# Kernel optimization log

Hardware: AMD Instinct MI355X
Metric: run time of the kernel (lower is better)

## Reference

```python
import jax, jax.numpy as jnp
import numpy as np

B, C_IN, N_NODES = 128, 64, 1024
N_TRIPLES = 3 * (N_NODES - 1)  # node 0 is the shared zero vector


def _btc(x, idx, w, b):
    # x: [B, C, N]; idx: [B, 3M]; w: [O, C, 3]; b: [O]
    Bv, C, _ = x.shape
    T = idx.shape[1]
    g = jnp.take_along_axis(x, jnp.broadcast_to(idx[:, None, :], (Bv, C, T)), axis=2)
    g = g.reshape(Bv, C, T // 3, 3)  # stride-3 kernel-3 conv == per-triple contraction
    out = jnp.einsum('bcnk,ock->bon', g, w) + b[None, :, None]
    zero = jnp.zeros((Bv, out.shape[1], 1), dtype=out.dtype)
    return jnp.concatenate([zero, out], axis=2)  # re-prepend zero node -> [B, O, N]


def _tln(x):
    mean = jnp.mean(x, axis=(1, 2), keepdims=True)
    std = jnp.std(x, axis=(1, 2), ddof=1, keepdims=True)  # torch.std is unbiased
    return (x - mean) / (std + 1e-5)


def _tower(x, idx, p):
    x = jax.nn.leaky_relu(_tln(_btc(x, idx, p['w_conv1'], p['b_conv1'])), 0.01)
    x = jax.nn.leaky_relu(_tln(_btc(x, idx, p['w_conv2'], p['b_conv2'])), 0.01)
    x = _tln(_btc(x, idx, p['w_conv3'], p['b_conv3']))
    x = jnp.max(x, axis=2)  # DynamicPooling -> [B, 64]
    x = jax.nn.leaky_relu(x @ p['w_fc1'].T + p['b_fc1'], 0.01)
    return x @ p['w_fc2'].T + p['b_fc2']  # [B, 1]  (Dropout is identity at eval)


def setup_inputs() -> dict:
    key = jax.random.key(0)
    ks = jax.random.split(key, 12)
    s = 0.05
    return {
        'data1': jax.random.normal(ks[0], (B, C_IN, N_NODES), jnp.float32),
        'idx1': jax.random.randint(ks[1], (B, N_TRIPLES, 1), 0, N_NODES, dtype=jnp.int64)
                if jax.config.jax_enable_x64 else
                jax.random.randint(ks[1], (B, N_TRIPLES, 1), 0, N_NODES).astype(jnp.int32),
        'data2': jax.random.normal(ks[2], (B, C_IN, N_NODES), jnp.float32),
        'idx2': jax.random.randint(ks[3], (B, N_TRIPLES, 1), 0, N_NODES).astype(jnp.int32),
        'w_conv1': jax.random.normal(ks[4], (256, C_IN, 3), jnp.float32) * s,
        'b_conv1': jnp.zeros((256,), jnp.float32),
        'w_conv2': jax.random.normal(ks[5], (128, 256, 3), jnp.float32) * s,
        'b_conv2': jnp.zeros((128,), jnp.float32),
        'w_conv3': jax.random.normal(ks[6], (64, 128, 3), jnp.float32) * s,
        'b_conv3': jnp.zeros((64,), jnp.float32),
        'w_fc1': jax.random.normal(ks[7], (32, 64), jnp.float32) * s,
        'b_fc1': jnp.zeros((32,), jnp.float32),
        'w_fc2': jax.random.normal(ks[8], (1, 32), jnp.float32) * s,
        'b_fc2': jnp.zeros((1,), jnp.float32),
    }


def reference(data1, idx1, data2, idx2,
              w_conv1, b_conv1, w_conv2, b_conv2, w_conv3, b_conv3,
              w_fc1, b_fc1, w_fc2, b_fc2):
    p = dict(w_conv1=w_conv1, b_conv1=b_conv1, w_conv2=w_conv2, b_conv2=b_conv2,
             w_conv3=w_conv3, b_conv3=b_conv3, w_fc1=w_fc1, b_fc1=b_fc1,
             w_fc2=w_fc2, b_fc2=b_fc2)
    y1 = _tower(data1, idx1[..., 0], p)
    y2 = _tower(data2, idx2[..., 0], p)
    return jnp.squeeze(jax.nn.sigmoid(y1 - y2), axis=1)  # [B]
```

## Files before the change

### kernel.cpp

```cpp
#include <hip/hip_runtime.h>
#include <math.h>

typedef __attribute__((ext_vector_type(8))) short short8;
typedef __attribute__((ext_vector_type(4))) float f32x4;
typedef __attribute__((ext_vector_type(2))) float f32x2;

#define LRELU(x) ((x) > 0.0f ? (x) : 0.01f * (x))

__device__ __forceinline__ float bf2f(unsigned short h) {
    return __uint_as_float(((unsigned int)h) << 16);
}
__device__ __forceinline__ unsigned short f2bf(float f) {
    unsigned int u = __float_as_uint(f);
    return (unsigned short)((u + 0x7FFFu + ((u >> 16) & 1u)) >> 16);
}
__device__ __forceinline__ unsigned int pack_bf16_pair(float lo, float hi) {
    unsigned int ul = __float_as_uint(lo) + 0x8000u;
    unsigned int uh = __float_as_uint(hi) + 0x8000u;
    return (ul >> 16) | (uh & 0xFFFF0000u);
}
__device__ __forceinline__ float2 stats_from(const float* sums, int b, float count) {
    float s = sums[2 * b], q = sums[2 * b + 1];
    float mean = s / count;
    float var = (q - s * s / count) / (count - 1.0f);
    var = fmaxf(var, 0.0f);
    return make_float2(mean, 1.0f / (sqrtf(var) + 1e-5f));
}
__device__ __forceinline__ void atomicMaxF(float* a, float v) {
    if (v >= 0.0f) atomicMax((int*)a, __float_as_int(v));
    else           atomicMin((unsigned int*)a, __float_as_uint(v));
}
__device__ __forceinline__ unsigned int norm_pair(unsigned int u, float a, float c) {
    f32x2 v;
    v.x = __uint_as_float(u << 16);
    v.y = __uint_as_float(u & 0xFFFF0000u);
    v = v * a + c;
    f32x2 m = v * 0.01f;
    v = __builtin_elementwise_max(v, m);
    return pack_bf16_pair(v.x, v.y);
}
__device__ __forceinline__ uint4 norm8(uint4 v, float a, float c) {
    v.x = norm_pair(v.x, a, c); v.y = norm_pair(v.y, a, c);
    v.z = norm_pair(v.z, a, c); v.w = norm_pair(v.w, a, c);
    return v;
}
__device__ __forceinline__ unsigned int fp8x4_nact(unsigned int u, float a, float c) {
    f32x2 lo = __builtin_amdgcn_cvt_pk_f32_fp8(u, false);
    f32x2 hi = __builtin_amdgcn_cvt_pk_f32_fp8(u, true);
    lo = lo * a + c; hi = hi * a + c;
    f32x2 ml = lo * 0.01f, mh = hi * 0.01f;
    lo = __builtin_elementwise_max(lo, ml);
    hi = __builtin_elementwise_max(hi, mh);
    int r = __builtin_amdgcn_cvt_pk_fp8_f32(lo.x, lo.y, 0, false);
    r = __builtin_amdgcn_cvt_pk_fp8_f32(hi.x, hi.y, r, true);
    return (unsigned int)r;
}

template <int MT, int WM>
__device__ __forceinline__ void mfma_step(const unsigned short* wt, const unsigned short* gt,
                                          f32x4 (&acc)[MT][4],
                                          int wo, int wn, int quad, int l15, int blkid)
{
#pragma unroll
    for (int st = 0; st < 2; ++st) {
        short8 af[MT], bfv[4];
        const int qb = st * 4 + quad;
#pragma unroll
        for (int i = 0; i < MT; i++) {
            const int orow = wo * WM + i * 16 + l15;
            af[i] = *(const short8*)&wt[orow * 64 + ((qb ^ blkid) << 3)];
        }
#pragma unroll
        for (int t = 0; t < 4; t++) {
            const int nrow = wn * 64 + t * 16 + l15;
            bfv[t] = *(const short8*)&gt[nrow * 64 + ((qb ^ blkid) << 3)];
        }
#pragma unroll
        for (int i = 0; i < MT; i++)
#pragma unroll
            for (int t = 0; t < 4; t++)
                acc[i][t] = __builtin_amdgcn_mfma_f32_16x16x32_bf16(
                    af[i], bfv[t], acc[i][t], 0, 0, 0);
    }
}

__global__ void prep_all(const float* __restrict__ w1, unsigned short* __restrict__ wq1,
                         const float* __restrict__ w2, unsigned char* __restrict__ wq2,
                         const float* __restrict__ w3, unsigned short* __restrict__ wq3)
{
    const int tid = blockIdx.x * blockDim.x + threadIdx.x;
    const int stride = gridDim.x * blockDim.x;
    for (int i = tid; i < 256 * 192; i += stride) {
        int o = i / 192, kp = i - o * 192;
        int j = kp >> 6, c = kp & 63;
        wq1[i] = f2bf(w1[(o * 64 + c) * 3 + j]);
    }
    for (int i = tid; i < (128 * 768) >> 2; i += stride) {
        const int e0 = i << 2;
        const int o = e0 / 768, kp0 = e0 - o * 768;
        const int j = kp0 >> 8, c0 = kp0 & 255;
        const float* src = &w2[(o * 256 + c0) * 3 + j];
        float f0 = src[0], f1 = src[3], f2 = src[6], f3 = src[9];
        int r = __builtin_amdgcn_cvt_pk_fp8_f32(f0, f1, 0, false);
        r = __builtin_amdgcn_cvt_pk_fp8_f32(f2, f3, r, true);
        *(unsigned int*)&wq2[e0] = (unsigned int)r;
    }
    for (int i = tid; i < 64 * 384; i += stride) {
        int o = i / 384, kp = i - o * 384;
        int j = kp >> 7, c = kp & 127;
        wq3[i] = f2bf(w3[(o * 128 + c) * 3 + j]);
    }
}

__global__ __launch_bounds__(256) void transpose_in(const float* __restrict__ inA,
                                                    const float* __restrict__ inB,
                                                    unsigned short* __restrict__ xT,
                                                    float* __restrict__ sums,
                                                    unsigned int* __restrict__ pmax)
{
    const int b = blockIdx.y, n0 = blockIdx.x * 64;
    const float* in = (b >= 128 ? inB : inA) + ((size_t)(b & 127) * 64) * 1024;
    const int tid = threadIdx.x;
    if (blockIdx.x == 0 && blockIdx.y == 0) {
        const int nBv = gridDim.y;
        for (int i = tid; i < 3 * nBv * 2; i += 256) sums[i] = 0.0f;
        for (int i = tid; i < nBv * 64; i += 256) pmax[i] = 0xFFFFFFFFu;
    }
    __shared__ float tile[64][65];
    const int nn = tid & 63, cw = tid >> 6;
#pragma unroll
    for (int i = 0; i < 16; i++) {
        int c = i * 4 + cw;
        tile[c][nn] = in[(size_t)c * 1024 + n0 + nn];
    }
    __syncthreads();
    const int n = tid >> 2, cp = (tid & 3) * 16;
    unsigned int pk[8];
#pragma unroll
    for (int i = 0; i < 8; i++) {
        unsigned short lo = f2bf(tile[cp + 2 * i][n]);
        unsigned short hi = f2bf(tile[cp + 2 * i + 1][n]);
        pk[i] = (unsigned int)lo | ((unsigned int)hi << 16);
    }
    unsigned short* dst = xT + ((size_t)b * 1024 + n0 + n) * 64 + cp;
    uint4 v0 = {pk[0], pk[1], pk[2], pk[3]};
    uint4 v1 = {pk[4], pk[5], pk[6], pk[7]};
    *(uint4*)dst = v0;
    *(uint4*)(dst + 8) = v1;
}

__global__ __launch_bounds__(256) void norm_act_fp8(unsigned char* __restrict__ a,
                                                    const float* __restrict__ sums,
                                                    float count)
{
    const int b = blockIdx.y;
    float2 st = stats_from(sums, b, count);
    const float na = st.y, nc = -st.x * st.y;
    uint4* p = (uint4*)(a + ((size_t)b << 18));
    const int base = blockIdx.x * 256 + threadIdx.x;
#pragma unroll
    for (int it = 0; it < 4; ++it) {
        const int idx = base + it * 4096;
        uint4 v = p[idx];
        v.x = fp8x4_nact(v.x, na, nc);
        v.y = fp8x4_nact(v.y, na, nc);
        v.z = fp8x4_nact(v.z, na, nc);
        v.w = fp8x4_nact(v.w, na, nc);
        p[idx] = v;
    }
}

template <int BM, bool POOL, bool NORM, bool FP8IN, bool FP8OUT>
__global__ __launch_bounds__(256, 3) void conv_mfma(
    const void* __restrict__ xTv,
    const int* __restrict__ idxA,
    const int* __restrict__ idxB,
    const unsigned short* __restrict__ wq,
    const float* __restrict__ bias,
    void* __restrict__ out,
    float* __restrict__ sums,
    float* __restrict__ pmax,
    const float* __restrict__ normSums,
    float normCount, int Cin, int cinShift, int O, int K)
{
    constexpr int WM = BM / 2, MT = WM / 16;
    constexpr int NW = (BM == 128) ? 4 : 2;
    const int b   = blockIdx.x;
    const int o0  = blockIdx.y * BM;
    const int nt0 = blockIdx.z << 7;
    const int tid = threadIdx.x;
    const int lane = tid & 63, wave = tid >> 6;
    const int wo = wave & 1, wn = wave >> 1;
    const int quad = lane >> 4, l15 = lane & 15;
    const int blkid = lane & 7;

    __shared__ __align__(16) unsigned short wt[BM * 64];
    __shared__ __align__(16) unsigned short gt[128 * 64];

    f32x4 acc[MT][4];
#pragma unroll
    for (int i = 0; i < MT; i++)
#pragma unroll
        for (int t = 0; t < 4; t++) acc[i][t] = (f32x4){0.f, 0.f, 0.f, 0.f};

    const unsigned short* xTb16 = (const unsigned short*)xTv + (((size_t)b) << 10) * (size_t)Cin;
    const unsigned char*  xTb8  = (const unsigned char*)xTv  + (((size_t)b) << 10) * (size_t)Cin;
    const int* idxb = (b >= 128 ? idxB : idxA) + (size_t)(b & 127) * 3069;

    float na = 1.0f, nc = 0.0f;
    if (NORM) {
        float2 st = stats_from(normSums, b, normCount);
        na = st.y; nc = -st.x * st.y;
    }

    const int gr = tid >> 1, gh = tid & 1;
    int s0, s1, s2;
    {
        int n = nt0 + gr;
        int t0 = (n == 0) ? 0 : (n - 1);
        s0 = idxb[3 * t0]; s1 = idxb[3 * t0 + 1]; s2 = idxb[3 * t0 + 2];
    }
    const int wr   = (BM == 128) ? (tid >> 1) : (tid >> 2);
    const int wseg = (BM == 128) ? (tid & 1) : (tid & 3);
    const unsigned short* wrow = wq + (size_t)(o0 + wr) * K + wseg * (NW * 8);
    const int gswz = gr & 7, wswz = wr & 7;

    uint4 g0A, g1A, g2A, g3A;
    uint4 g0B, g1B, g2B, g3B;

#define LOADC(S, KC) {                                                           \
        const int k64_ = (KC) << 6;                                              \
        const int j_   = k64_ >> cinShift;                                       \
        const int c0_  = k64_ & (Cin - 1);                                       \
        const int src_ = (j_ == 0) ? s0 : ((j_ == 1) ? s1 : s2);                 \
        if (FP8IN) {                                                             \
            const uint4* gp_ = (const uint4*)(xTb8 + (size_t)src_ * Cin + c0_ + gh * 32); \
            g0##S = gp_[0]; g1##S = gp_[1];                                      \
        } else {                                                                 \
            const uint4* gp_ = (const uint4*)(xTb16 + (size_t)src_ * Cin + c0_ + gh * 32); \
            g0##S = gp_[0]; g1##S = gp_[1]; g2##S = gp_[2]; g3##S = gp_[3];      \
        }                                                                        \
    }

#define STAGE(S, KC) {                                                           \
        const uint4* wp_ = (const uint4*)(wrow + ((KC) << 6));                   \
        uint4 wv0 = wp_[0], wv1 = wp_[1], wv2, wv3;                              \
        if (NW == 4) { wv2 = wp_[2]; wv3 = wp_[3]; }                             \
        uint4 h0, h1, h2, h3;                                                    \
        h0 = g0##S; h1 = g1##S; h2 = g2##S; h3 = g3##S;                          \
        if (NORM) {                                                              \
            h0 = norm8(h0, na, nc); h1 = norm8(h1, na, nc);                      \
            h2 = norm8(h2, na, nc); h3 = norm8(h3, na, nc);                      \
        }                                                                        \
        *(uint4*)&gt[gr * 64 + (((gh << 2) | 0) ^ gswz) * 8] = h0;               \
        *(uint4*)&gt[gr * 64 + (((gh << 2) | 1) ^ gswz) * 8] = h1;               \
        *(uint4*)&gt[gr * 64 + (((gh << 2) | 2) ^ gswz) * 8] = h2;               \
        *(uint4*)&gt[gr * 64 + (((gh << 2) | 3) ^ gswz) * 8] = h3;               \
        *(uint4*)&wt[wr * 64 + ((wseg * NW + 0) ^ wswz) * 8] = wv0;              \
        *(uint4*)&wt[wr * 64 + ((wseg * NW + 1) ^ wswz) * 8] = wv1;              \
        if (NW == 4) {                                                           \
            *(uint4*)&wt[wr * 64 + ((wseg * NW + 2) ^ wswz) * 8] = wv2;          \
            *(uint4*)&wt[wr * 64 + ((wseg * NW + 3) ^ wswz) * 8] = wv3;          \
        }                                                                        \
    }

    const int nChunks = K >> 6;
    LOADC(A, 0);
    if (nChunks > 1) LOADC(B, 1);
    int kc = 0;
    for (; kc + 2 <= nChunks; kc += 2) {
        if (kc) __syncthreads();
        STAGE(A, kc);
        if (kc + 2 < nChunks) LOADC(A, kc + 2);
        __syncthreads();
        mfma_step<MT, WM>(wt, gt, acc, wo, wn, quad, l15, blkid);
        __syncthreads();
        STAGE(B, kc + 1);
        if (kc + 3 < nChunks) LOADC(B, kc + 3);
        __syncthreads();
        mfma_step<MT, WM>(wt, gt, acc, wo, wn, quad, l15, blkid);
    }
    if (kc < nChunks) {
        __syncthreads();
        STAGE(A, kc);
        __syncthreads();
        mfma_step<MT, WM>(wt, gt, acc, wo, wn, quad, l15, blkid);
    }
#undef LOADC
#undef STAGE

    float lsum = 0.f, lsq = 0.f;
#pragma unroll
    for (int i = 0; i < MT; i++) {
        const int ob = o0 + wo * WM + i * 16 + quad * 4;
        const float4 bv = *(const float4*)(bias + ob);
        float mx0 = -1e30f, mx1 = -1e30f, mx2 = -1e30f, mx3 = -1e30f;
#pragma unroll
        for (int t = 0; t < 4; t++) {
            const int n = nt0 + wn * 64 + t * 16 + l15;
            float v0 = acc[i][t][0] + bv.x;
            float v1 = acc[i][t][1] + bv.y;
            float v2 = acc[i][t][2] + bv.z;
            float v3 = acc[i][t][3] + bv.w;
            if (n == 0) { v0 = v1 = v2 = v3 = 0.f; }
            lsum += v0 + v1 + v2 + v3;
            lsq  += v0 * v0 + v1 * v1 + v2 * v2 + v3 * v3;
            if (POOL) {
                mx0 = fmaxf(mx0, v0); mx1 = fmaxf(mx1, v1);
                mx2 = fmaxf(mx2, v2); mx3 = fmaxf(mx3, v3);
            } else if (FP8OUT) {
                int r = __builtin_amdgcn_cvt_pk_fp8_f32(v0, v1, 0, false);
                r = __builtin_amdgcn_cvt_pk_fp8_f32(v2, v3, r, true);
                *(unsigned int*)&((unsigned char*)out)[((size_t)b * 1024 + n) * O + ob] =
                    (unsigned int)r;
            } else {
                uint2 pk;
                pk.x = pack_bf16_pair(v0, v1);
                pk.y = pack_bf16_pair(v2, v3);
                *(uint2*)&((unsigned short*)out)[((size_t)b * 1024 + n) * O + ob] = pk;
            }
        }
        if (POOL) {
#pragma unroll
            for (int off = 1; off < 16; off <<= 1) {
                mx0 = fmaxf(mx0, __shfl_xor(mx0, off));
                mx1 = fmaxf(mx1, __shfl_xor(mx1, off));
                mx2 = fmaxf(mx2, __shfl_xor(mx2, off));
                mx3 = fmaxf(mx3, __shfl_xor(mx3, off));
            }
            if (l15 == 0) {
                atomicMaxF(&pmax[(size_t)b * 64 + ob + 0], mx0);
                atomicMaxF(&pmax[(size_t)b * 64 + ob + 1], mx1);
                atomicMaxF(&pmax[(size_t)b * 64 + ob + 2], mx2);
                atomicMaxF(&pmax[(size_t)b * 64 + ob + 3], mx3);
            }
        }
    }
#pragma unroll
    for (int off = 32; off > 0; off >>= 1) {
        lsum += __shfl_down(lsum, off);
        lsq  += __shfl_down(lsq, off);
    }
    float* red = (float*)wt;
    if (lane == 0) { red[wave] = lsum; red[4 + wave] = lsq; }
    __syncthreads();
    if (tid == 0) {
        atomicAdd(&sums[2 * b + 0], red[0] + red[1] + red[2] + red[3]);
        atomicAdd(&sums[2 * b + 1], red[4] + red[5] + red[6] + red[7]);
    }
}

__global__ __launch_bounds__(256, 3) void conv2_fp8(
    const unsigned char* __restrict__ a1,
    const int* __restrict__ idxA,
    const int* __restrict__ idxB,
    const unsigned char* __restrict__ wq8,
    const float* __restrict__ bias,
    unsigned short* __restrict__ out,
    float* __restrict__ sums)
{
    const int b   = blockIdx.x;
    const int nt0 = blockIdx.z << 7;
    const int tid = threadIdx.x;
    const int lane = tid & 63, wave = tid >> 6;
    const int wo = wave & 1, wn = wave >> 1;
    const int quad = lane >> 4, l15 = lane & 15;
    const int blkid = lane & 7;

    __shared__ __align__(16) unsigned char wt8[128 * 128];
    __shared__ __align__(16) unsigned char gt8[128 * 128];

    f32x4 acc[4][4];
#pragma unroll
    for (int i = 0; i < 4; i++)
#pragma unroll
        for (int t = 0; t < 4; t++) acc[i][t] = (f32x4){0.f, 0.f, 0.f, 0.f};

    const unsigned char* xb = a1 + (((size_t)b) << 10) * 256;
    const int* idxb = (b >= 128 ? idxB : idxA) + (size_t)(b & 127) * 3069;

    const int gr = tid >> 1, gh = tid & 1;
    int si0, si1, si2;
    {
        int n = nt0 + gr;
        int t0 = (n == 0) ? 0 : (n - 1);
        si0 = idxb[3 * t0]; si1 = idxb[3 * t0 + 1]; si2 = idxb[3 * t0 + 2];
    }
    const unsigned char* wrow = wq8 + (size_t)gr * 768 + gh * 64;
    const int swz = gr & 7;

    uint4 g0A, g1A, g2A, g3A;
    uint4 g0B, g1B, g2B, g3B;

#define LOADC2(S, KC) {                                                          \
        const int j_  = (KC) >> 1;                                               \
        const int c0_ = ((KC) & 1) << 7;                                         \
        const int src_ = (j_ == 0) ? si0 : ((j_ == 1) ? si1 : si2);              \
        const uint4* gp_ = (const uint4*)(xb + (size_t)src_ * 256 + c0_ + gh * 64); \
        g0##S = gp_[0]; g1##S = gp_[1]; g2##S = gp_[2]; g3##S = gp_[3];          \
    }

#define STAGE2(S, KC) {                                                          \
        const uint4* wp_ = (const uint4*)(wrow + (KC) * 128);                    \
        uint4 wv0 = wp_[0], wv1 = wp_[1], wv2 = wp_[2], wv3 = wp_[3];            \
        *(uint4*)&gt8[gr * 128 + (((gh << 2) | 0) ^ swz) * 16] = g0##S;          \
        *(uint4*)&gt8[gr * 128 + (((gh << 2) | 1) ^ swz) * 16] = g1##S;          \
        *(uint4*)&gt8[gr * 128 + (((gh << 2) | 2) ^ swz) * 16] = g2##S;          \
        *(uint4*)&gt8[gr * 128 + (((gh << 2) | 3) ^ swz) * 16] = g3##S;          \
        *(uint4*)&wt8[gr * 128 + (((gh << 2) | 0) ^ swz) * 16] = wv0;            \
        *(uint4*)&wt8[gr * 128 + (((gh << 2) | 1) ^ swz) * 16] = wv1;            \
        *(uint4*)&wt8[gr * 128 + (((gh << 2) | 2) ^ swz) * 16] = wv2;            \
        *(uint4*)&wt8[gr * 128 + (((gh << 2) | 3) ^ swz) * 16] = wv3;            \
    }

#define MFMA_STEP2 {                                                             \
        _Pragma("unroll")                                                        \
        for (int st = 0; st < 4; ++st) {                                         \
            long af0, af1, af2, af3, bf0, bf1, bf2, bf3;                         \
            const int qb = st * 4 + quad;                                        \
            const int cg = qb >> 1, ch = (qb & 1) << 3;                          \
            {                                                                    \
                const int r0 = wo * 64 + 0 * 16 + l15;                           \
                af0 = *(const long*)&wt8[r0 * 128 + ((cg ^ blkid) << 4) + ch];   \
                const int r1 = wo * 64 + 1 * 16 + l15;                           \
                af1 = *(const long*)&wt8[r1 * 128 + ((cg ^ blkid) << 4) + ch];   \
                const int r2 = wo * 64 + 2 * 16 + l15;                           \
                af2 = *(const long*)&wt8[r2 * 128 + ((cg ^ blkid) << 4) + ch];   \
                const int r3 = wo * 64 + 3 * 16 + l15;                           \
                af3 = *(const long*)&wt8[r3 * 128 + ((cg ^ blkid) << 4) + ch];   \
                const int n0 = wn * 64 + 0 * 16 + l15;                           \
                bf0 = *(const long*)&gt8[n0 * 128 + ((cg ^ blkid) << 4) + ch];   \
                const int n1 = wn * 64 + 1 * 16 + l15;                           \
                bf1 = *(const long*)&gt8[n1 * 128 + ((cg ^ blkid) << 4) + ch];   \
                const int n2 = wn * 64 + 2 * 16 + l15;                           \
                bf2 = *(const long*)&gt8[n2 * 128 + ((cg ^ blkid) << 4) + ch];   \
                const int n3 = wn * 64 + 3 * 16 + l15;                           \
                bf3 = *(const long*)&gt8[n3 * 128 + ((cg ^ blkid) << 4) + ch];   \
            }                                                                    \
            acc[0][0] = __builtin_amdgcn_mfma_f32_16x16x32_fp8_fp8(af0, bf0, acc[0][0], 0, 0, 0); \
            acc[0][1] = __builtin_amdgcn_mfma_f32_16x16x32_fp8_fp8(af0, bf1, acc[0][1], 0, 0, 0); \
            acc[0][2] = __builtin_amdgcn_mfma_f32_16x16x32_fp8_fp8(af0, bf2, acc[0][2], 0, 0, 0); \
            acc[0][3] = __builtin_amdgcn_mfma_f32_16x16x32_fp8_fp8(af0, bf3, acc[0][3], 0, 0, 0); \
            acc[1][0] = __builtin_amdgcn_mfma_f32_16x16x32_fp8_fp8(af1, bf0, acc[1][0], 0, 0, 0); \
            acc[1][1] = __builtin_amdgcn_mfma_f32_16x16x32_fp8_fp8(af1, bf1, acc[1][1], 0, 0, 0); \
            acc[1][2] = __builtin_amdgcn_mfma_f32_16x16x32_fp8_fp8(af1, bf2, acc[1][2], 0, 0, 0); \
            acc[1][3] = __builtin_amdgcn_mfma_f32_16x16x32_fp8_fp8(af1, bf3, acc[1][3], 0, 0, 0); \
            acc[2][0] = __builtin_amdgcn_mfma_f32_16x16x32_fp8_fp8(af2, bf0, acc[2][0], 0, 0, 0); \
            acc[2][1] = __builtin_amdgcn_mfma_f32_16x16x32_fp8_fp8(af2, bf1, acc[2][1], 0, 0, 0); \
            acc[2][2] = __builtin_amdgcn_mfma_f32_16x16x32_fp8_fp8(af2, bf2, acc[2][2], 0, 0, 0); \
            acc[2][3] = __builtin_amdgcn_mfma_f32_16x16x32_fp8_fp8(af2, bf3, acc[2][3], 0, 0, 0); \
            acc[3][0] = __builtin_amdgcn_mfma_f32_16x16x32_fp8_fp8(af3, bf0, acc[3][0], 0, 0, 0); \
            acc[3][1] = __builtin_amdgcn_mfma_f32_16x16x32_fp8_fp8(af3, bf1, acc[3][1], 0, 0, 0); \
            acc[3][2] = __builtin_amdgcn_mfma_f32_16x16x32_fp8_fp8(af3, bf2, acc[3][2], 0, 0, 0); \
            acc[3][3] = __builtin_amdgcn_mfma_f32_16x16x32_fp8_fp8(af3, bf3, acc[3][3], 0, 0, 0); \
        }                                                                        \
    }

    LOADC2(A, 0);
    LOADC2(B, 1);
    int kc = 0;
    for (; kc + 2 <= 6; kc += 2) {
        if (kc) __syncthreads();
        STAGE2(A, kc);
        if (kc + 2 < 6) LOADC2(A, kc + 2);
        __syncthreads();
        MFMA_STEP2;
        __syncthreads();
        STAGE2(B, kc + 1);
        if (kc + 3 < 6) LOADC2(B, kc + 3);
        __syncthreads();
        MFMA_STEP2;
    }
#undef LOADC2
#undef STAGE2
#undef MFMA_STEP2

    float lsum = 0.f, lsq = 0.f;
#pragma unroll
    for (int i = 0; i < 4; i++) {
        const int ob = wo * 64 + i * 16 + quad * 4;
        const float4 bv = *(const float4*)(bias + ob);
#pragma unroll
        for (int t = 0; t < 4; t++) {
            const int n = nt0 + wn * 64 + t * 16 + l15;
            float v0 = acc[i][t][0] + bv.x;
            float v1 = acc[i][t][1] + bv.y;
            float v2 = acc[i][t][2] + bv.z;
            float v3 = acc[i][t][3] + bv.w;
            if (n == 0) { v0 = v1 = v2 = v3 = 0.f; }
            lsum += v0 + v1 + v2 + v3;
            lsq  += v0 * v0 + v1 * v1 + v2 * v2 + v3 * v3;
            uint2 pk;
            pk.x = pack_bf16_pair(v0, v1);
            pk.y = pack_bf16_pair(v2, v3);
            *(uint2*)&out[((size_t)b * 1024 + n) * 128 + ob] = pk;
        }
    }
#pragma unroll
    for (int off = 32; off > 0; off >>= 1) {
        lsum += __shfl_down(lsum, off);
        lsq  += __shfl_down(lsq, off);
    }
    float* red = (float*)wt8;
    if (lane == 0) { red[wave] = lsum; red[4 + wave] = lsq; }
    __syncthreads();
    if (tid == 0) {
        atomicAdd(&sums[2 * b + 0], red[0] + red[1] + red[2] + red[3]);
        atomicAdd(&sums[2 * b + 1], red[4] + red[5] + red[6] + red[7]);
    }
}

__global__ __launch_bounds__(64) void fc_head(
    const float* __restrict__ pmax, const float* __restrict__ sums3, float count,
    const float* __restrict__ w_fc1, const float* __restrict__ b_fc1,
    const float* __restrict__ w_fc2, const float* __restrict__ b_fc2,
    float* __restrict__ y)
{
    const int b = blockIdx.x, t = threadIdx.x;
    __shared__ float pooled[64];
    __shared__ float hid[32];
    float2 s = stats_from(sums3, b, count);
    pooled[t] = (pmax[(size_t)b * 64 + t] - s.x) * s.y;
    __syncthreads();
    if (t < 32) {
        float h = b_fc1[t];
#pragma unroll
        for (int c = 0; c < 64; c++) h += pooled[c] * w_fc1[t * 64 + c];
        hid[t] = LRELU(h);
    }
    __syncthreads();
    if (t == 0) {
        float v = b_fc2[0];
#pragma unroll
        for (int c = 0; c < 32; c++) v += hid[c] * w_fc2[c];
        y[b] = v;
    }
}

__global__ void sigmoid_diff(const float* __restrict__ y1,
                             const float* __restrict__ y2,
                             float* __restrict__ out)
{
    int b = threadIdx.x;
    if (b < 128) out[b] = 1.0f / (1.0f + expf(-(y1[b] - y2[b])));
}

extern "C" void kernel_launch(void* const* d_in, const int* in_sizes, int n_in,
                              void* d_out, int out_size, void* d_ws, size_t ws_size,
                              hipStream_t stream)
{
    const float* data1 = (const float*)d_in[0];
    const int*   idx1  = (const int*)d_in[1];
    const float* data2 = (const float*)d_in[2];
    const int*   idx2  = (const int*)d_in[3];
    const float* w1 = (const float*)d_in[4];
    const float* b1 = (const float*)d_in[5];
    const float* w2 = (const float*)d_in[6];
    const float* b2 = (const float*)d_in[7];
    const float* w3 = (const float*)d_in[8];
    const float* b3 = (const float*)d_in[9];
    const float* wfc1 = (const float*)d_in[10];
    const float* bfc1 = (const float*)d_in[11];
    const float* wfc2 = (const float*)d_in[12];
    const float* bfc2 = (const float*)d_in[13];

    const size_t needM = (size_t)256 * 1024 * (64 * 2 + 256 * 1 + 128 * 2) + 768 * 1024;
    const bool merged = ws_size >= needM;
    const int nB = merged ? 256 : 128;
    const size_t szXT = (size_t)nB * 1024 * 64 * 2;
    const size_t szA1 = (size_t)nB * 1024 * 256;
    const size_t szA2 = (size_t)nB * 1024 * 128 * 2;

    char* ws = (char*)d_ws;
    unsigned short* xT = (unsigned short*)ws;
    unsigned char*  a1 = (unsigned char*)(ws + szXT);
    unsigned short* a2 = (unsigned short*)(ws + szXT + szA1);
    char* tail = ws + szXT + szA1 + szA2;
    unsigned short* wq1 = (unsigned short*)tail;
    unsigned char*  wq2f8 = (unsigned char*)(tail + 128 * 1024);
    unsigned short* wq3 = (unsigned short*)(tail + 384 * 1024);
    float* sums = (float*)(tail + 448 * 1024);
    float* pmax = (float*)(tail + 512 * 1024);
    float* yv   = (float*)(tail + 640 * 1024);

    prep_all<<<96, 256, 0, stream>>>(w1, wq1, w2, wq2f8, w3, wq3);

    const int nIter = merged ? 1 : 2;
    for (int t = 0; t < nIter; ++t) {
        const float* dA = (merged || t == 0) ? data1 : data2;
        const float* dB = merged ? data2 : dA;
        const int* iA = (merged || t == 0) ? idx1 : idx2;
        const int* iB = merged ? idx2 : iA;
        float* s1 = sums;
        float* s2 = sums + nB * 2;
        float* s3 = sums + nB * 4;

        transpose_in<<<dim3(16, nB), 256, 0, stream>>>(dA, dB, xT, sums,
                                                       (unsigned int*)pmax);

        conv_mfma<128, false, false, false, true><<<dim3(nB, 2, 8), 256, 0, stream>>>(
            xT, iA, iB, wq1, b1, a1, s1, nullptr, nullptr, 0.0f, 64, 6, 256, 192);

        norm_act_fp8<<<dim3(16, nB), 256, 0, stream>>>(a1, s1, 256.0f * 1024.0f);

        conv2_fp8<<<dim3(nB, 1, 8), 256, 0, stream>>>(
            a1, iA, iB, wq2f8, b2, a2, s2);

        conv_mfma<64, true, true, false, false><<<dim3(nB, 1, 8), 256, 0, stream>>>(
            a2, iA, iB, wq3, b3, nullptr, s3, pmax, s2, 128.0f * 1024.0f, 128, 7, 64, 384);

        fc_head<<<nB, 64, 0, stream>>>(pmax, s3, 64.0f * 1024.0f,
                                       wfc1, bfc1, wfc2, bfc2,
                                       yv + (merged ? 0 : t * 128));
    }
    sigmoid_diff<<<1, 128, 0, stream>>>(yv, yv + 128, (float*)d_out);
}
```

Before: 318.1 us.

## Move conv3 to FP8 with separate norm pass and LDS-staged coalesced epilogue stores

Converts the conv2 output activations and conv3 weights to FP8. A separate norm_act_fp8 pass now normalises conv2's output, and a new dedicated conv3_fp8 kernel uses fp8 MFMA. The conv1 and conv2 epilogues now stage outputs through swizzled LDS and write coalesced 16-byte rows instead of scattered 4/8-byte stores. Index triples are loaded as one Int3. This halves the a2 traffic and speeds up conv3's MFMA, at the cost of an extra kernel launch and lower precision in conv3's inputs and weights.

```diff
diff --git a/kernel.cpp b/kernel.cpp
--- a/kernel.cpp
+++ b/kernel.cpp
@@ -7,9 +7,8 @@
 
 #define LRELU(x) ((x) > 0.0f ? (x) : 0.01f * (x))
 
-__device__ __forceinline__ float bf2f(unsigned short h) {
-    return __uint_as_float(((unsigned int)h) << 16);
-}
+struct __align__(4) Int3 { int x, y, z; };
+
 __device__ __forceinline__ unsigned short f2bf(float f) {
     unsigned int u = __float_as_uint(f);
     return (unsigned short)((u + 0x7FFFu + ((u >> 16) & 1u)) >> 16);
@@ -29,20 +28,6 @@
 __device__ __forceinline__ void atomicMaxF(float* a, float v) {
     if (v >= 0.0f) atomicMax((int*)a, __float_as_int(v));
     else           atomicMin((unsigned int*)a, __float_as_uint(v));
-}
-__device__ __forceinline__ unsigned int norm_pair(unsigned int u, float a, float c) {
-    f32x2 v;
-    v.x = __uint_as_float(u << 16);
-    v.y = __uint_as_float(u & 0xFFFF0000u);
-    v = v * a + c;
-    f32x2 m = v * 0.01f;
-    v = __builtin_elementwise_max(v, m);
-    return pack_bf16_pair(v.x, v.y);
-}
-__device__ __forceinline__ uint4 norm8(uint4 v, float a, float c) {
-    v.x = norm_pair(v.x, a, c); v.y = norm_pair(v.y, a, c);
-    v.z = norm_pair(v.z, a, c); v.w = norm_pair(v.w, a, c);
-    return v;
 }
 __device__ __forceinline__ unsigned int fp8x4_nact(unsigned int u, float a, float c) {
     f32x2 lo = __builtin_amdgcn_cvt_pk_f32_fp8(u, false);
@@ -86,7 +71,7 @@
 
 __global__ void prep_all(const float* __restrict__ w1, unsigned short* __restrict__ wq1,
                          const float* __restrict__ w2, unsigned char* __restrict__ wq2,
-                         const float* __restrict__ w3, unsigned short* __restrict__ wq3)
+                         const float* __restrict__ w3, unsigned char* __restrict__ wq3)
 {
     const int tid = blockIdx.x * blockDim.x + threadIdx.x;
     const int stride = gridDim.x * blockDim.x;
@@ -105,10 +90,15 @@
         r = __builtin_amdgcn_cvt_pk_fp8_f32(f2, f3, r, true);
         *(unsigned int*)&wq2[e0] = (unsigned int)r;
     }
-    for (int i = tid; i < 64 * 384; i += stride) {
-        int o = i / 384, kp = i - o * 384;
-        int j = kp >> 7, c = kp & 127;
-        wq3[i] = f2bf(w3[(o * 128 + c) * 3 + j]);
+    for (int i = tid; i < (64 * 384) >> 2; i += stride) {
+        const int e0 = i << 2;
+        const int o = e0 / 384, kp0 = e0 - o * 384;
+        const int j = kp0 >> 7, c0 = kp0 & 127;
+        const float* src = &w3[(o * 128 + c0) * 3 + j];
+        float f0 = src[0], f1 = src[3], f2 = src[6], f3 = src[9];
+        int r = __builtin_amdgcn_cvt_pk_fp8_f32(f0, f1, 0, false);
+        r = __builtin_amdgcn_cvt_pk_fp8_f32(f2, f3, r, true);
+        *(unsigned int*)&wq3[e0] = (unsigned int)r;
     }
 }
 
@@ -151,16 +141,13 @@
 
 __global__ __launch_bounds__(256) void norm_act_fp8(unsigned char* __restrict__ a,
                                                     const float* __restrict__ sums,
-                                                    float count)
+                                                    float count, int u4PerB)
 {
     const int b = blockIdx.y;
     float2 st = stats_from(sums, b, count);
     const float na = st.y, nc = -st.x * st.y;
-    uint4* p = (uint4*)(a + ((size_t)b << 18));
-    const int base = blockIdx.x * 256 + threadIdx.x;
-#pragma unroll
-    for (int it = 0; it < 4; ++it) {
-        const int idx = base + it * 4096;
+    uint4* p = (uint4*)a + (size_t)b * u4PerB;
+    for (int idx = blockIdx.x * 256 + threadIdx.x; idx < u4PerB; idx += gridDim.x * 256) {
         uint4 v = p[idx];
         v.x = fp8x4_nact(v.x, na, nc);
         v.y = fp8x4_nact(v.y, na, nc);
@@ -170,23 +157,17 @@
     }
 }
 
-template <int BM, bool POOL, bool NORM, bool FP8IN, bool FP8OUT>
-__global__ __launch_bounds__(256, 3) void conv_mfma(
-    const void* __restrict__ xTv,
+__global__ __launch_bounds__(256, 3) void conv1_mfma(
+    const unsigned short* __restrict__ xT,
     const int* __restrict__ idxA,
     const int* __restrict__ idxB,
     const unsigned short* __restrict__ wq,
     const float* __restrict__ bias,
-    void* __restrict__ out,
-    float* __restrict__ sums,
-    float* __restrict__ pmax,
-    const float* __restrict__ normSums,
-    float normCount, int Cin, int cinShift, int O, int K)
-{
-    constexpr int WM = BM / 2, MT = WM / 16;
-    constexpr int NW = (BM == 128) ? 4 : 2;
+    unsigned char* __restrict__ out,
+    float* __restrict__ sums)
+{
     const int b   = blockIdx.x;
-    const int o0  = blockIdx.y * BM;
+    const int o0  = blockIdx.y * 128;
     const int nt0 = blockIdx.z << 7;
     const int tid = threadIdx.x;
     const int lane = tid & 63, wave = tid >> 6;
@@ -194,146 +175,95 @@
     const int quad = lane >> 4, l15 = lane & 15;
     const int blkid = lane & 7;
 
-    __shared__ __align__(16) unsigned short wt[BM * 64];
+    __shared__ __align__(16) unsigned short wt[128 * 64];
     __shared__ __align__(16) unsigned short gt[128 * 64];
 
-    f32x4 acc[MT][4];
-#pragma unroll
-    for (int i = 0; i < MT; i++)
+    f32x4 acc[4][4];
+#pragma unroll
+    for (int i = 0; i < 4; i++)
 #pragma unroll
         for (int t = 0; t < 4; t++) acc[i][t] = (f32x4){0.f, 0.f, 0.f, 0.f};
 
-    const unsigned short* xTb16 = (const unsigned short*)xTv + (((size_t)b) << 10) * (size_t)Cin;
-    const unsigned char*  xTb8  = (const unsigned char*)xTv  + (((size_t)b) << 10) * (size_t)Cin;
+    const unsigned short* xTb = xT + (((size_t)b) << 10) * 64;
     const int* idxb = (b >= 128 ? idxB : idxA) + (size_t)(b & 127) * 3069;
-
-    float na = 1.0f, nc = 0.0f;
-    if (NORM) {
-        float2 st = stats_from(normSums, b, normCount);
-        na = st.y; nc = -st.x * st.y;
-    }
 
     const int gr = tid >> 1, gh = tid & 1;
     int s0, s1, s2;
     {
         int n = nt0 + gr;
         int t0 = (n == 0) ? 0 : (n - 1);
-        s0 = idxb[3 * t0]; s1 = idxb[3 * t0 + 1]; s2 = idxb[3 * t0 + 2];
-    }
-    const int wr   = (BM == 128) ? (tid >> 1) : (tid >> 2);
-    const int wseg = (BM == 128) ? (tid & 1) : (tid & 3);
-    const unsigned short* wrow = wq + (size_t)(o0 + wr) * K + wseg * (NW * 8);
+        const Int3 sv = *(const Int3*)&idxb[3 * t0];
+        s0 = sv.x; s1 = sv.y; s2 = sv.z;
+    }
+    const int wr = tid >> 1, wseg = tid & 1;
+    const unsigned short* wrow = wq + (size_t)(o0 + wr) * 192 + wseg * 32;
     const int gswz = gr & 7, wswz = wr & 7;
 
     uint4 g0A, g1A, g2A, g3A;
     uint4 g0B, g1B, g2B, g3B;
 
 #define LOADC(S, KC) {                                                           \
-        const int k64_ = (KC) << 6;                                              \
-        const int j_   = k64_ >> cinShift;                                       \
-        const int c0_  = k64_ & (Cin - 1);                                       \
-        const int src_ = (j_ == 0) ? s0 : ((j_ == 1) ? s1 : s2);                 \
-        if (FP8IN) {                                                             \
-            const uint4* gp_ = (const uint4*)(xTb8 + (size_t)src_ * Cin + c0_ + gh * 32); \
-            g0##S = gp_[0]; g1##S = gp_[1];                                      \
-        } else {                                                                 \
-            const uint4* gp_ = (const uint4*)(xTb16 + (size_t)src_ * Cin + c0_ + gh * 32); \
-            g0##S = gp_[0]; g1##S = gp_[1]; g2##S = gp_[2]; g3##S = gp_[3];      \
-        }                                                                        \
+        const int src_ = ((KC) == 0) ? s0 : (((KC) == 1) ? s1 : s2);             \
+        const uint4* gp_ = (const uint4*)(xTb + (size_t)src_ * 64 + gh * 32);    \
+        g0##S = gp_[0]; g1##S = gp_[1]; g2##S = gp_[2]; g3##S = gp_[3];          \
     }
 
 #define STAGE(S, KC) {                                                           \
         const uint4* wp_ = (const uint4*)(wrow + ((KC) << 6));                   \
-        uint4 wv0 = wp_[0], wv1 = wp_[1], wv2, wv3;                              \
-        if (NW == 4) { wv2 = wp_[2]; wv3 = wp_[3]; }                             \
-        uint4 h0, h1, h2, h3;                                                    \
-        h0 = g0##S; h1 = g1##S; h2 = g2##S; h3 = g3##S;                          \
-        if (NORM) {                                                              \
-            h0 = norm8(h0, na, nc); h1 = norm8(h1, na, nc);                      \
-            h2 = norm8(h2, na, nc); h3 = norm8(h3, na, nc);                      \
-        }                                                                        \
-        *(uint4*)&gt[gr * 64 + (((gh << 2) | 0) ^ gswz) * 8] = h0;               \
-        *(uint4*)&gt[gr * 64 + (((gh << 2) | 1) ^ gswz) * 8] = h1;               \
-        *(uint4*)&gt[gr * 64 + (((gh << 2) | 2) ^ gswz) * 8] = h2;               \
-        *(uint4*)&gt[gr * 64 + (((gh << 2) | 3) ^ gswz) * 8] = h3;               \
-        *(uint4*)&wt[wr * 64 + ((wseg * NW + 0) ^ wswz) * 8] = wv0;              \
-        *(uint4*)&wt[wr * 64 + ((wseg * NW + 1) ^ wswz) * 8] = wv1;              \
-        if (NW == 4) {                                                           \
-            *(uint4*)&wt[wr * 64 + ((wseg * NW + 2) ^ wswz) * 8] = wv2;          \
-            *(uint4*)&wt[wr * 64 + ((wseg * NW + 3) ^ wswz) * 8] = wv3;          \
-        }                                                                        \
-    }
-
-    const int nChunks = K >> 6;
+        uint4 wv0 = wp_[0], wv1 = wp_[1], wv2 = wp_[2], wv3 = wp_[3];            \
+        *(uint4*)&gt[gr * 64 + (((gh << 2) | 0) ^ gswz) * 8] = g0##S;            \
+        *(uint4*)&gt[gr * 64 + (((gh << 2) | 1) ^ gswz) * 8] = g1##S;            \
+        *(uint4*)&gt[gr * 64 + (((gh << 2) | 2) ^ gswz) * 8] = g2##S;            \
+        *(uint4*)&gt[gr * 64 + (((gh << 2) | 3) ^ gswz) * 8] = g3##S;            \
+        *(uint4*)&wt[wr * 64 + ((wseg * 4 + 0) ^ wswz) * 8] = wv0;               \
+        *(uint4*)&wt[wr * 64 + ((wseg * 4 + 1) ^ wswz) * 8] = wv1;               \
+        *(uint4*)&wt[wr * 64 + ((wseg * 4 + 2) ^ wswz) * 8] = wv2;               \
+        *(uint4*)&wt[wr * 64 + ((wseg * 4 + 3) ^ wswz) * 8] = wv3;               \
+    }
+
     LOADC(A, 0);
-    if (nChunks > 1) LOADC(B, 1);
+    LOADC(B, 1);
     int kc = 0;
-    for (; kc + 2 <= nChunks; kc += 2) {
+    for (; kc + 2 <= 3; kc += 2) {
         if (kc) __syncthreads();
         STAGE(A, kc);
-        if (kc + 2 < nChunks) LOADC(A, kc + 2);
-        __syncthreads();
-        mfma_step<MT, WM>(wt, gt, acc, wo, wn, quad, l15, blkid);
+        if (kc + 2 < 3) LOADC(A, kc + 2);
+        __syncthreads();
+        mfma_step<4, 64>(wt, gt, acc, wo, wn, quad, l15, blkid);
         __syncthreads();
         STAGE(B, kc + 1);
-        if (kc + 3 < nChunks) LOADC(B, kc + 3);
-        __syncthreads();
-        mfma_step<MT, WM>(wt, gt, acc, wo, wn, quad, l15, blkid);
-    }
-    if (kc < nChunks) {
-        __syncthreads();
-        STAGE(A, kc);
-        __syncthreads();
-        mfma_step<MT, WM>(wt, gt, acc, wo, wn, quad, l15, blkid);
+        __syncthreads();
+        mfma_step<4, 64>(wt, gt, acc, wo, wn, quad, l15, blkid);
+    }
+    {
+        __syncthreads();
+        STAGE(A, 2);
+        __syncthreads();
+        mfma_step<4, 64>(wt, gt, acc, wo, wn, quad, l15, blkid);
     }
 #undef LOADC
 #undef STAGE
 
+    __syncthreads();
+    unsigned char* eb = (unsigned char*)gt;
     float lsum = 0.f, lsq = 0.f;
 #pragma unroll
-    for (int i = 0; i < MT; i++) {
-        const int ob = o0 + wo * WM + i * 16 + quad * 4;
-        const float4 bv = *(const float4*)(bias + ob);
-        float mx0 = -1e30f, mx1 = -1e30f, mx2 = -1e30f, mx3 = -1e30f;
+    for (int i = 0; i < 4; i++) {
+        const int obl = wo * 64 + i * 16 + quad * 4;
+        const float4 bv = *(const float4*)(bias + o0 + obl);
 #pragma unroll
         for (int t = 0; t < 4; t++) {
-            const int n = nt0 + wn * 64 + t * 16 + l15;
+            const int nl = wn * 64 + t * 16 + l15;
             float v0 = acc[i][t][0] + bv.x;
             float v1 = acc[i][t][1] + bv.y;
             float v2 = acc[i][t][2] + bv.z;
             float v3 = acc[i][t][3] + bv.w;
-            if (n == 0) { v0 = v1 = v2 = v3 = 0.f; }
+            if (nt0 + nl == 0) { v0 = v1 = v2 = v3 = 0.f; }
             lsum += v0 + v1 + v2 + v3;
             lsq  += v0 * v0 + v1 * v1 + v2 * v2 + v3 * v3;
-            if (POOL) {
-                mx0 = fmaxf(mx0, v0); mx1 = fmaxf(mx1, v1);
-                mx2 = fmaxf(mx2, v2); mx3 = fmaxf(mx3, v3);
-            } else if (FP8OUT) {
-                int r = __builtin_amdgcn_cvt_pk_fp8_f32(v0, v1, 0, false);
-                r = __builtin_amdgcn_cvt_pk_fp8_f32(v2, v3, r, true);
-                *(unsigned int*)&((unsigned char*)out)[((size_t)b * 1024 + n) * O + ob] =
-                    (unsigned int)r;
-            } else {
-                uint2 pk;
-                pk.x = pack_bf16_pair(v0, v1);
-                pk.y = pack_bf16_pair(v2, v3);
-                *(uint2*)&((unsigned short*)out)[((size_t)b * 1024 + n) * O + ob] = pk;
-            }
-        }
-        if (POOL) {
-#pragma unroll
-            for (int off = 1; off < 16; off <<= 1) {
-                mx0 = fmaxf(mx0, __shfl_xor(mx0, off));
-                mx1 = fmaxf(mx1, __shfl_xor(mx1, off));
-                mx2 = fmaxf(mx2, __shfl_xor(mx2, off));
-                mx3 = fmaxf(mx3, __shfl_xor(mx3, off));
-            }
-            if (l15 == 0) {
-                atomicMaxF(&pmax[(size_t)b * 64 + ob + 0], mx0);
-                atomicMaxF(&pmax[(size_t)b * 64 + ob + 1], mx1);
-                atomicMaxF(&pmax[(size_t)b * 64 + ob + 2], mx2);
-                atomicMaxF(&pmax[(size_t)b * 64 + ob + 3], mx3);
-            }
+            int r = __builtin_amdgcn_cvt_pk_fp8_f32(v0, v1, 0, false);
+            r = __builtin_amdgcn_cvt_pk_fp8_f32(v2, v3, r, true);
+            *(unsigned int*)&eb[nl * 128 + (obl ^ ((nl & 7) << 4))] = (unsigned int)r;
         }
     }
 #pragma unroll
@@ -344,6 +274,13 @@
     float* red = (float*)wt;
     if (lane == 0) { red[wave] = lsum; red[4 + wave] = lsq; }
     __syncthreads();
+#pragma unroll
+    for (int c = 0; c < 4; ++c) {
+        const int ch = c * 256 + tid;
+        const int row = ch >> 3, off = (ch & 7) << 4;
+        uint4 v = *(const uint4*)&eb[row * 128 + (off ^ ((row & 7) << 4))];
+        *(uint4*)&out[((size_t)b * 1024 + nt0 + row) * 256 + o0 + off] = v;
+    }
     if (tid == 0) {
         atomicAdd(&sums[2 * b + 0], red[0] + red[1] + red[2] + red[3]);
         atomicAdd(&sums[2 * b + 1], red[4] + red[5] + red[6] + red[7]);
@@ -356,7 +293,7 @@
     const int* __restrict__ idxB,
     const unsigned char* __restrict__ wq8,
     const float* __restrict__ bias,
-    unsigned short* __restrict__ out,
+    unsigned char* __restrict__ out,
     float* __restrict__ sums)
 {
     const int b   = blockIdx.x;
@@ -384,7 +321,8 @@
     {
         int n = nt0 + gr;
         int t0 = (n == 0) ? 0 : (n - 1);
-        si0 = idxb[3 * t0]; si1 = idxb[3 * t0 + 1]; si2 = idxb[3 * t0 + 2];
+        const Int3 sv = *(const Int3*)&idxb[3 * t0];
+        si0 = sv.x; si1 = sv.y; si2 = sv.z;
     }
     const unsigned char* wrow = wq8 + (size_t)gr * 768 + gh * 64;
     const int swz = gr & 7;
@@ -475,11 +413,172 @@
 #undef STAGE2
 #undef MFMA_STEP2
 
+    __syncthreads();
+    unsigned char* eb = gt8;
     float lsum = 0.f, lsq = 0.f;
 #pragma unroll
     for (int i = 0; i < 4; i++) {
-        const int ob = wo * 64 + i * 16 + quad * 4;
+        const int obl = wo * 64 + i * 16 + quad * 4;
+        const float4 bv = *(const float4*)(bias + obl);
+#pragma unroll
+        for (int t = 0; t < 4; t++) {
+            const int nl = wn * 64 + t * 16 + l15;
+            float v0 = acc[i][t][0] + bv.x;
+            float v1 = acc[i][t][1] + bv.y;
+            float v2 = acc[i][t][2] + bv.z;
+            float v3 = acc[i][t][3] + bv.w;
+            if (nt0 + nl == 0) { v0 = v1 = v2 = v3 = 0.f; }
+            lsum += v0 + v1 + v2 + v3;
+            lsq  += v0 * v0 + v1 * v1 + v2 * v2 + v3 * v3;
+            int r = __builtin_amdgcn_cvt_pk_fp8_f32(v0, v1, 0, false);
+            r = __builtin_amdgcn_cvt_pk_fp8_f32(v2, v3, r, true);
+            *(unsigned int*)&eb[nl * 128 + (obl ^ ((nl & 7) << 4))] = (unsigned int)r;
+        }
+    }
+#pragma unroll
+    for (int off = 32; off > 0; off >>= 1) {
+        lsum += __shfl_down(lsum, off);
+        lsq  += __shfl_down(lsq, off);
+    }
+    float* red = (float*)wt8;
+    if (lane == 0) { red[wave] = lsum; red[4 + wave] = lsq; }
+    __syncthreads();
+#pragma unroll
+    for (int c = 0; c < 4; ++c) {
+        const int ch = c * 256 + tid;
+        const int row = ch >> 3, off = (ch & 7) << 4;
+        uint4 v = *(const uint4*)&eb[row * 128 + (off ^ ((row & 7) << 4))];
+        *(uint4*)&out[((size_t)b * 1024 + nt0 + row) * 128 + off] = v;
+    }
+    if (tid == 0) {
+        atomicAdd(&sums[2 * b + 0], red[0] + red[1] + red[2] + red[3]);
+        atomicAdd(&sums[2 * b + 1], red[4] + red[5] + red[6] + red[7]);
+    }
+}
+
+__global__ __launch_bounds__(256, 3) void conv3_fp8(
+    const unsigned char* __restrict__ a2,
+    const int* __restrict__ idxA,
+    const int* __restrict__ idxB,
+    const unsigned char* __restrict__ wq8,
+    const float* __restrict__ bias,
+    float* __restrict__ sums,
+    float* __restrict__ pmax)
+{
+    const int b   = blockIdx.x;
+    const int nt0 = blockIdx.z << 7;
+    const int tid = threadIdx.x;
+    const int lane = tid & 63, wave = tid >> 6;
+    const int wo = wave & 1, wn = wave >> 1;
+    const int quad = lane >> 4, l15 = lane & 15;
+    const int blkid = lane & 7;
+
+    __shared__ __align__(16) unsigned char wt8[64 * 128];
+    __shared__ __align__(16) unsigned char gt8[128 * 128];
+
+    f32x4 acc[2][4];
+#pragma unroll
+    for (int i = 0; i < 2; i++)
+#pragma unroll
+        for (int t = 0; t < 4; t++) acc[i][t] = (f32x4){0.f, 0.f, 0.f, 0.f};
+
+    const unsigned char* xb = a2 + (((size_t)b) << 10) * 128;
+    const int* idxb = (b >= 128 ? idxB : idxA) + (size_t)(b & 127) * 3069;
+
+    const int gr = tid >> 1, gh = tid & 1;
+    int si0, si1, si2;
+    {
+        int n = nt0 + gr;
+        int t0 = (n == 0) ? 0 : (n - 1);
+        const Int3 sv = *(const Int3*)&idxb[3 * t0];
+        si0 = sv.x; si1 = sv.y; si2 = sv.z;
+    }
+    const int wr = tid >> 2, wseg = tid & 3;
+    const unsigned char* wrow = wq8 + (size_t)wr * 384 + wseg * 32;
+    const int gswz = gr & 7, wswz = wr & 7;
+
+    uint4 g0A, g1A, g2A, g3A;
+    uint4 g0B, g1B, g2B, g3B;
+
+#define LOADC3(S, KC) {                                                          \
+        const int src_ = ((KC) == 0) ? si0 : (((KC) == 1) ? si1 : si2);          \
+        const uint4* gp_ = (const uint4*)(xb + (size_t)src_ * 128 + gh * 64);    \
+        g0##S = gp_[0]; g1##S = gp_[1]; g2##S = gp_[2]; g3##S = gp_[3];          \
+    }
+
+#define STAGE3(S, KC) {                                                          \
+        const uint4* wp_ = (const uint4*)(wrow + (KC) * 128);                    \
+        uint4 wv0 = wp_[0], wv1 = wp_[1];                                        \
+        *(uint4*)&gt8[gr * 128 + (((gh << 2) | 0) ^ gswz) * 16] = g0##S;         \
+        *(uint4*)&gt8[gr * 128 + (((gh << 2) | 1) ^ gswz) * 16] = g1##S;         \
+        *(uint4*)&gt8[gr * 128 + (((gh << 2) | 2) ^ gswz) * 16] = g2##S;         \
+        *(uint4*)&gt8[gr * 128 + (((gh << 2) | 3) ^ gswz) * 16] = g3##S;         \
+        *(uint4*)&wt8[wr * 128 + (((wseg << 1) | 0) ^ wswz) * 16] = wv0;         \
+        *(uint4*)&wt8[wr * 128 + (((wseg << 1) | 1) ^ wswz) * 16] = wv1;         \
+    }
+
+#define MFMA_STEP3 {                                                             \
+        _Pragma("unroll")                                                        \
+        for (int st = 0; st < 4; ++st) {                                         \
+            long af0, af1, bf0, bf1, bf2, bf3;                                   \
+            const int qb = st * 4 + quad;                                        \
+            const int cg = qb >> 1, ch = (qb & 1) << 3;                          \
+            {                                                                    \
+                const int r0 = wo * 32 + 0 * 16 + l15;                           \
+                af0 = *(const long*)&wt8[r0 * 128 + ((cg ^ blkid) << 4) + ch];   \
+                const int r1 = wo * 32 + 1 * 16 + l15;                           \
+                af1 = *(const long*)&wt8[r1 * 128 + ((cg ^ blkid) << 4) + ch];   \
+                const int n0 = wn * 64 + 0 * 16 + l15;                           \
+                bf0 = *(const long*)&gt8[n0 * 128 + ((cg ^ blkid) << 4) + ch];   \
+                const int n1 = wn * 64 + 1 * 16 + l15;                           \
+                bf1 = *(const long*)&gt8[n1 * 128 + ((cg ^ blkid) << 4) + ch];   \
+                const int n2 = wn * 64 + 2 * 16 + l15;                           \
+                bf2 = *(const long*)&gt8[n2 * 128 + ((cg ^ blkid) << 4) + ch];   \
+                const int n3 = wn * 64 + 3 * 16 + l15;                           \
+                bf3 = *(const long*)&gt8[n3 * 128 + ((cg ^ blkid) << 4) + ch];   \
+            }                                                                    \
+            acc[0][0] = __builtin_amdgcn_mfma_f32_16x16x32_fp8_fp8(af0, bf0, acc[0][0], 0, 0, 0); \
+            acc[0][1] = __builtin_amdgcn_mfma_f32_16x16x32_fp8_fp8(af0, bf1, acc[0][1], 0, 0, 0); \
+            acc[0][2] = __builtin_amdgcn_mfma_f32_16x16x32_fp8_fp8(af0, bf2, acc[0][2], 0, 0, 0); \
+            acc[0][3] = __builtin_amdgcn_mfma_f32_16x16x32_fp8_fp8(af0, bf3, acc[0][3], 0, 0, 0); \
+            acc[1][0] = __builtin_amdgcn_mfma_f32_16x16x32_fp8_fp8(af1, bf0, acc[1][0], 0, 0, 0); \
+            acc[1][1] = __builtin_amdgcn_mfma_f32_16x16x32_fp8_fp8(af1, bf1, acc[1][1], 0, 0, 0); \
+            acc[1][2] = __builtin_amdgcn_mfma_f32_16x16x32_fp8_fp8(af1, bf2, acc[1][2], 0, 0, 0); \
+            acc[1][3] = __builtin_amdgcn_mfma_f32_16x16x32_fp8_fp8(af1, bf3, acc[1][3], 0, 0, 0); \
+        }                                                                        \
+    }
+
+    LOADC3(A, 0);
+    LOADC3(B, 1);
+    int kc = 0;
+    for (; kc + 2 <= 3; kc += 2) {
+        if (kc) __syncthreads();
+        STAGE3(A, kc);
+        if (kc + 2 < 3) LOADC3(A, kc + 2);
+        __syncthreads();
+        MFMA_STEP3;
+        __syncthreads();
+        STAGE3(B, kc + 1);
+        __syncthreads();
+        MFMA_STEP3;
+    }
+    {
+        __syncthreads();
+        STAGE3(A, 2);
+        __syncthreads();
+        MFMA_STEP3;
+    }
+#undef LOADC3
+#undef STAGE3
+#undef MFMA_STEP3
+
+    __syncthreads();
+    float lsum = 0.f, lsq = 0.f;
+#pragma unroll
+    for (int i = 0; i < 2; i++) {
+        const int ob = wo * 32 + i * 16 + quad * 4;
         const float4 bv = *(const float4*)(bias + ob);
+        float mx0 = -1e30f, mx1 = -1e30f, mx2 = -1e30f, mx3 = -1e30f;
 #pragma unroll
         for (int t = 0; t < 4; t++) {
             const int n = nt0 + wn * 64 + t * 16 + l15;
@@ -490,10 +589,21 @@
             if (n == 0) { v0 = v1 = v2 = v3 = 0.f; }
             lsum += v0 + v1 + v2 + v3;
             lsq  += v0 * v0 + v1 * v1 + v2 * v2 + v3 * v3;
-            uint2 pk;
-            pk.x = pack_bf16_pair(v0, v1);
-            pk.y = pack_bf16_pair(v2, v3);
-            *(uint2*)&out[((size_t)b * 1024 + n) * 128 + ob] = pk;
+            mx0 = fmaxf(mx0, v0); mx1 = fmaxf(mx1, v1);
+            mx2 = fmaxf(mx2, v2); mx3 = fmaxf(mx3, v3);
+        }
+#pragma unroll
+        for (int off = 1; off < 16; off <<= 1) {
+            mx0 = fmaxf(mx0, __shfl_xor(mx0, off));
+            mx1 = fmaxf(mx1, __shfl_xor(mx1, off));
+            mx2 = fmaxf(mx2, __shfl_xor(mx2, off));
+            mx3 = fmaxf(mx3, __shfl_xor(mx3, off));
+        }
+        if (l15 == 0) {
+            atomicMaxF(&pmax[(size_t)b * 64 + ob + 0], mx0);
+            atomicMaxF(&pmax[(size_t)b * 64 + ob + 1], mx1);
+            atomicMaxF(&pmax[(size_t)b * 64 + ob + 2], mx2);
+            atomicMaxF(&pmax[(size_t)b * 64 + ob + 3], mx3);
         }
     }
 #pragma unroll
@@ -564,26 +674,26 @@
     const float* wfc2 = (const float*)d_in[12];
     const float* bfc2 = (const float*)d_in[13];
 
-    const size_t needM = (size_t)256 * 1024 * (64 * 2 + 256 * 1 + 128 * 2) + 768 * 1024;
+    const size_t needM = (size_t)256 * 1024 * (64 * 2 + 256 * 1 + 128 * 1) + 768 * 1024;
     const bool merged = ws_size >= needM;
     const int nB = merged ? 256 : 128;
     const size_t szXT = (size_t)nB * 1024 * 64 * 2;
     const size_t szA1 = (size_t)nB * 1024 * 256;
-    const size_t szA2 = (size_t)nB * 1024 * 128 * 2;
+    const size_t szA2 = (size_t)nB * 1024 * 128;
 
     char* ws = (char*)d_ws;
     unsigned short* xT = (unsigned short*)ws;
     unsigned char*  a1 = (unsigned char*)(ws + szXT);
-    unsigned short* a2 = (unsigned short*)(ws + szXT + szA1);
+    unsigned char*  a2 = (unsigned char*)(ws + szXT + szA1);
     char* tail = ws + szXT + szA1 + szA2;
-    unsigned short* wq1 = (unsigned short*)tail;
+    unsigned short* wq1   = (unsigned short*)tail;
     unsigned char*  wq2f8 = (unsigned char*)(tail + 128 * 1024);
-    unsigned short* wq3 = (unsigned short*)(tail + 384 * 1024);
+    unsigned char*  wq3f8 = (unsigned char*)(tail + 384 * 1024);
     float* sums = (float*)(tail + 448 * 1024);
     float* pmax = (float*)(tail + 512 * 1024);
     float* yv   = (float*)(tail + 640 * 1024);
 
-    prep_all<<<96, 256, 0, stream>>>(w1, wq1, w2, wq2f8, w3, wq3);
+    prep_all<<<96, 256, 0, stream>>>(w1, wq1, w2, wq2f8, w3, wq3f8);
 
     const int nIter = merged ? 1 : 2;
     for (int t = 0; t < nIter; ++t) {
@@ -598,16 +708,18 @@
         transpose_in<<<dim3(16, nB), 256, 0, stream>>>(dA, dB, xT, sums,
                                                        (unsigned int*)pmax);
 
-        conv_mfma<128, false, false, false, true><<<dim3(nB, 2, 8), 256, 0, stream>>>(
-            xT, iA, iB, wq1, b1, a1, s1, nullptr, nullptr, 0.0f, 64, 6, 256, 192);
-
-        norm_act_fp8<<<dim3(16, nB), 256, 0, stream>>>(a1, s1, 256.0f * 1024.0f);
+        conv1_mfma<<<dim3(nB, 2, 8), 256, 0, stream>>>(
+            xT, iA, iB, wq1, b1, a1, s1);
+
+        norm_act_fp8<<<dim3(16, nB), 256, 0, stream>>>(a1, s1, 256.0f * 1024.0f, 16384);
 
         conv2_fp8<<<dim3(nB, 1, 8), 256, 0, stream>>>(
             a1, iA, iB, wq2f8, b2, a2, s2);
 
-        conv_mfma<64, true, true, false, false><<<dim3(nB, 1, 8), 256, 0, stream>>>(
-            a2, iA, iB, wq3, b3, nullptr, s3, pmax, s2, 128.0f * 1024.0f, 128, 7, 64, 384);
+        norm_act_fp8<<<dim3(8, nB), 256, 0, stream>>>(a2, s2, 128.0f * 1024.0f, 8192);
+
+        conv3_fp8<<<dim3(nB, 1, 8), 256, 0, stream>>>(
+            a2, iA, iB, wq3f8, b3, s3, pmax);
 
         fc_head<<<nB, 64, 0, stream>>>(pmax, s3, 64.0f * 1024.0f,
                                        wfc1, bfc1, wfc2, bfc2,
```

Result: faster. 281.6 us (-11.5%).
